# Optimization experiments

Hardware: AMD Instinct MI355X
Metric: run time of the kernel (lower is better)

Reference implementation:

```python
import jax, jax.numpy as jnp
import numpy as np

NH, NL, NP, GA = 8, 4, 4, 8  # num_heads, num_levels, num_points, grid_align_num
SHAPES = np.array([[128, 128], [64, 64], [32, 32], [16, 16]], dtype=np.int64)  # (W, H) per level


def _grid_sample(img, grid):
    """F.grid_sample bilinear, padding_mode='zeros', align_corners=False.
    img: [N,C,H,W], grid: [N,Hg,Wg,2] in [-1,1] (x,y). Returns [N,C,Hg,Wg]."""
    N, C, H, W = img.shape
    x = (grid[..., 0] + 1.0) * (W * 0.5) - 0.5
    y = (grid[..., 1] + 1.0) * (H * 0.5) - 0.5
    x0 = jnp.floor(x)
    y0 = jnp.floor(y)
    wx = (x - x0)[:, None]  # [N,1,Hg,Wg]
    wy = (y - y0)[:, None]
    x0i = x0.astype(jnp.int32)
    y0i = y0.astype(jnp.int32)
    img_flat = img.reshape(N, C, H * W)
    Hg, Wg = grid.shape[1], grid.shape[2]

    def tap(ix, iy):
        valid = (ix >= 0) & (ix < W) & (iy >= 0) & (iy < H)
        lin = jnp.clip(iy, 0, H - 1) * W + jnp.clip(ix, 0, W - 1)
        v = jnp.take_along_axis(img_flat, lin.reshape(N, 1, Hg * Wg), axis=2)
        return v.reshape(N, C, Hg, Wg) * valid[:, None].astype(img.dtype)

    v00 = tap(x0i, y0i)
    v01 = tap(x0i + 1, y0i)
    v10 = tap(x0i, y0i + 1)
    v11 = tap(x0i + 1, y0i + 1)
    return (v00 * (1 - wx) * (1 - wy) + v01 * wx * (1 - wy)
            + v10 * (1 - wx) * wy + v11 * wx * wy)


def setup_inputs() -> dict:
    key = jax.random.key(0)
    ks = jax.random.split(key, 6)
    bs, nq, E = 2, 16384, 256
    total = int((SHAPES[:, 0] * SHAPES[:, 1]).sum())  # 21760
    query = jax.random.normal(ks[0], (bs, nq, E), jnp.float32)
    value = jax.random.normal(ks[1], (bs, total, NH, E // NH), jnp.float32)
    reference_points = jax.random.uniform(ks[2], (bs, nq, 1, NL * 2), jnp.float32)
    W_off = jax.random.normal(ks[3], (NH * NL * NP * 2, E), jnp.float32) * 0.01
    # structured offset bias per init_weights (directional rays, radius ~ point index)
    thetas = jnp.arange(NH, dtype=jnp.float32) * (2.0 * np.pi / NH)
    gi = jnp.stack([jnp.cos(thetas), jnp.sin(thetas)], -1)  # [NH,2]
    gi = gi / jnp.max(jnp.abs(gi), axis=-1, keepdims=True)
    gi = jnp.tile(gi[:, None, None, :], (1, NL, NP, 1))
    gi = gi * jnp.arange(1, NP + 1, dtype=jnp.float32)[None, None, :, None]
    b_off = gi.reshape(-1)
    W_attn = jax.random.normal(ks[4], (NH * NL * NP, E), jnp.float32) * 0.01
    b_attn = jax.random.normal(ks[5], (NH * NL * NP,), jnp.float32) * 0.01
    return {"query": query, "value": value, "reference_points": reference_points,
            "W_off": W_off, "b_off": b_off, "W_attn": W_attn, "b_attn": b_attn,
            "spatial_shapes": np.asarray(SHAPES)}


def reference(query, value, reference_points, W_off, b_off, W_attn, b_attn, spatial_shapes):
    bs, nq, E = query.shape
    d = E // NH
    shapes = np.asarray(spatial_shapes)  # static [L,2] (W,H)

    # sampling offsets and locations (non-deploy path)
    off = (query @ W_off.T + b_off).reshape(bs, nq, NH, NL * NP * 2)
    ref = jnp.tile(reference_points, (1, 1, NH, NP)).reshape(bs, nq, NH, NL * NP * 2)
    # offset_normalizer: (1/spatial_shapes).repeat(1, NP).flatten() -> layout (l, p, xy)
    norm = jnp.asarray(np.tile(1.0 / shapes.astype(np.float32), (1, NP)).reshape(-1))
    loc = (ref + off * norm) * 2.0 - 1.0  # [bs, nq, NH, NL*NP*2]

    # attention weights: softmax over levels*points, regrouped to (L, G, P) layout
    attn = jax.nn.softmax((query @ W_attn.T + b_attn).reshape(bs, nq, NH, NL * NP), axis=-1)
    attn = (attn.reshape(bs, nq // GA, GA, NH, NL, NP)
            .transpose(0, 3, 1, 4, 2, 5)
            .reshape(bs * NH, 1, nq // GA, NL * GA * NP))

    grids = loc.reshape(bs, nq, NH, NL, NP, 2)
    outs = []
    start = 0
    for lvl in range(NL):
        W_, H_ = int(shapes[lvl, 0]), int(shapes[lvl, 1])
        n = H_ * W_
        v = value[:, start:start + n].transpose(0, 2, 3, 1).reshape(bs * NH, d, H_, W_)
        start += n
        g = grids[:, :, :, lvl].transpose(0, 2, 1, 3, 4).reshape(bs * NH, nq // GA, GA * NP, 2)
        outs.append(_grid_sample(v, g))  # [bs*NH, d, nq//GA, GA*NP]
    samp = jnp.concatenate(outs, axis=-1) * attn  # [bs*NH, d, nq//GA, NL*GA*NP]
    # reduce_sum linear with fixed 0/1 weight == sum over levels and points per group slot
    out = samp.reshape(bs * NH, d, nq // GA, NL, GA, NP).sum(axis=(3, 5))
    return out.reshape(bs, NH * d, nq)
```

## Files before the change

kernel.cpp:

```cpp
#include <hip/hip_runtime.h>
#include <hip/hip_bf16.h>


typedef __attribute__((ext_vector_type(4))) float    float4v;
typedef __attribute__((ext_vector_type(8))) _Float16 half8;
typedef __attribute__((ext_vector_type(4))) _Float16 half4;

#define NQ    16384
#define NTOK  21760
#define NLOG  384

#define N_V4  2785280
#define N_W4  24576

__global__ __launch_bounds__(256) void convert_kernel(
    const float* __restrict__ val,
    const float* __restrict__ Woff, const float* __restrict__ Wattn,
    _Float16* __restrict__ vh, _Float16* __restrict__ wh) {
  int i = blockIdx.x * 256 + threadIdx.x;
  float4v v;
  half4* dst;
  if (i < N_V4) {
    v = ((const float4v*)val)[i];
    dst = ((half4*)vh) + i;
  } else {
    int j = i - N_V4;
    int n = j >> 6;
    int k4 = j & 63;
    const float* src = (n < 256) ? (Woff + (size_t)n * 256)
                                 : (Wattn + (size_t)(n - 256) * 256);
    v = *(const float4v*)(src + k4 * 4);
    dst = ((half4*)wh) + j;
  }
  half4 o;
  o[0] = (_Float16)v[0]; o[1] = (_Float16)v[1];
  o[2] = (_Float16)v[2]; o[3] = (_Float16)v[3];
  *dst = o;
}

#define LDSTR 88
__global__ __launch_bounds__(256) void gemm_kernel(
    const float* __restrict__ qf, const _Float16* __restrict__ wh,
    const float* __restrict__ boff, const float* __restrict__ battn,
    float* __restrict__ logits) {
  __shared__ _Float16 As[128 * LDSTR];
  __shared__ _Float16 Bs[128 * LDSTR];

  const int tid  = threadIdx.x;
  const int lane = tid & 63;
  const int wv   = tid >> 6;
  const int wm   = wv >> 1, wn = wv & 1;
  const int quad = lane >> 4;
  const int r    = lane & 15;
  const int blockM = blockIdx.x * 128;
  const int n0     = blockIdx.y * 128;

  float4v acc[4][4];
#pragma unroll
  for (int i = 0; i < 4; ++i)
#pragma unroll
    for (int j = 0; j < 4; ++j) acc[i][j] = (float4v){0.f, 0.f, 0.f, 0.f};

  for (int kc = 0; kc < 4; ++kc) {
    const int k0 = kc * 64;
    if (kc) __syncthreads();
#pragma unroll
    for (int it = 0; it < 8; ++it) {
      int idx = it * 256 + tid;
      int row = idx >> 4, k4 = idx & 15;
      float4v v = *(const float4v*)(qf + (size_t)(blockM + row) * 256 + k0 + k4 * 4);
      half4 o;
      o[0] = (_Float16)v[0]; o[1] = (_Float16)v[1];
      o[2] = (_Float16)v[2]; o[3] = (_Float16)v[3];
      *(half4*)&As[row * LDSTR + k4 * 4] = o;
    }
#pragma unroll
    for (int it = 0; it < 4; ++it) {
      int idx = it * 256 + tid;
      int row = idx >> 3, c8 = idx & 7;
      *(half8*)&Bs[row * LDSTR + c8 * 8] =
          *(const half8*)(wh + (size_t)(n0 + row) * 256 + k0 + c8 * 8);
    }
    __syncthreads();

#pragma unroll
    for (int kf = 0; kf < 2; ++kf) {
      const int ko = kf * 32 + quad * 8;
      half8 af[4], bf[4];
#pragma unroll
      for (int mi = 0; mi < 4; ++mi)
        af[mi] = *(const half8*)&As[(wm * 64 + mi * 16 + r) * LDSTR + ko];
#pragma unroll
      for (int ni = 0; ni < 4; ++ni)
        bf[ni] = *(const half8*)&Bs[(wn * 64 + ni * 16 + r) * LDSTR + ko];
#pragma unroll
      for (int mi = 0; mi < 4; ++mi)
#pragma unroll
        for (int ni = 0; ni < 4; ++ni)
          acc[mi][ni] = __builtin_amdgcn_mfma_f32_16x16x32_f16(af[mi], bf[ni], acc[mi][ni], 0, 0, 0);
    }
  }

#pragma unroll
  for (int mi = 0; mi < 4; ++mi) {
    const int mb = blockM + wm * 64 + mi * 16 + quad * 4;
#pragma unroll
    for (int ni = 0; ni < 4; ++ni) {
      const int n = n0 + wn * 64 + ni * 16 + r;
      const float bias = (n < 256) ? boff[n] : battn[n - 256];
#pragma unroll
      for (int reg = 0; reg < 4; ++reg)
        logits[(size_t)(mb + reg) * NLOG + n] = acc[mi][ni][reg] + bias;
    }
  }
}

__global__ __launch_bounds__(256) void sample_kernel(
    const _Float16* __restrict__ vh, const float* __restrict__ refp,
    const float* __restrict__ logits, float* __restrict__ out) {
  const int qt = blockIdx.x, h = blockIdx.y, b = blockIdx.z;
  const int tid = threadIdx.x;
  const int c4 = tid & 3;
  const int qi = tid >> 2;
  const int q  = qt * 64 + qi;
  const size_t bq = (size_t)b * NQ + q;
  const float* lg = logits + bq * NLOG;

  float4v al4[4];
#pragma unroll
  for (int i = 0; i < 4; ++i)
    al4[i] = *(const float4v*)(lg + 256 + h * 16 + i * 4);
  float mx = -1e30f;
#pragma unroll
  for (int i = 0; i < 4; ++i)
#pragma unroll
    for (int j = 0; j < 4; ++j) mx = fmaxf(mx, al4[i][j]);
  float ssum = 0.f;
#pragma unroll
  for (int i = 0; i < 4; ++i)
#pragma unroll
    for (int j = 0; j < 4; ++j) {
      float e = __expf(al4[i][j] - mx);
      al4[i][j] = e;
      ssum += e;
    }
  const float inv = 1.0f / ssum;

  float4v offv[8];
#pragma unroll
  for (int i = 0; i < 8; ++i)
    offv[i] = *(const float4v*)(lg + h * 32 + i * 4);
  float4v rp0 = *(const float4v*)(refp + bq * 8);
  float4v rp1 = *(const float4v*)(refp + bq * 8 + 4);
  const float rpx[4] = {rp0[0], rp0[2], rp1[0], rp1[2]};
  const float rpy[4] = {rp0[1], rp0[3], rp1[1], rp1[3]};

  const _Float16* vb = vh + (size_t)b * NTOK * 256 + h * 32 + c4 * 8;
  float4v acc0 = (float4v){0.f, 0.f, 0.f, 0.f};
  float4v acc1 = (float4v){0.f, 0.f, 0.f, 0.f};

  const int base[4] = {0, 16384, 20480, 21504};

#pragma unroll
  for (int l = 0; l < 4; ++l) {
    const int   W  = 128 >> l;
    const float fW = (float)W;
    const _Float16* vlev = vb + (size_t)base[l] * 256;
#pragma unroll
    for (int p = 0; p < 4; ++p) {
      const float a  = al4[l][p] * inv;
      const float ox = offv[l * 2 + (p >> 1)][(p & 1) * 2];
      const float oy = offv[l * 2 + (p >> 1)][(p & 1) * 2 + 1];
      const float x = rpx[p] * fW + ox - 0.5f;
      const float y = rpy[p] * fW + oy - 0.5f;
      const float xf = floorf(x), yf = floorf(y);
      const float fx = x - xf, fy = y - yf;
      const int ix = (int)xf, iy = (int)yf;
      const int ix0 = min(max(ix, 0), W - 1);
      const int ix1 = min(max(ix + 1, 0), W - 1);
      const int iy0 = min(max(iy, 0), W - 1);
      const int iy1 = min(max(iy + 1, 0), W - 1);
      const float wx0 = ((unsigned)ix       < (unsigned)W) ? 1.f - fx : 0.f;
      const float wx1 = ((unsigned)(ix + 1) < (unsigned)W) ? fx       : 0.f;
      const float wy0 = ((unsigned)iy       < (unsigned)W) ? 1.f - fy : 0.f;
      const float wy1 = ((unsigned)(iy + 1) < (unsigned)W) ? fy       : 0.f;
      const float w00 = a * wx0 * wy0, w01 = a * wx1 * wy0;
      const float w10 = a * wx0 * wy1, w11 = a * wx1 * wy1;
      const _Float16* r0 = vlev + (size_t)(iy0 * W) * 256;
      const _Float16* r1 = vlev + (size_t)(iy1 * W) * 256;
      half8 t00 = *(const half8*)(r0 + ix0 * 256);
      half8 t01 = *(const half8*)(r0 + ix1 * 256);
      half8 t10 = *(const half8*)(r1 + ix0 * 256);
      half8 t11 = *(const half8*)(r1 + ix1 * 256);
#pragma unroll
      for (int j = 0; j < 4; ++j) {
        acc0[j] += w00 * (float)t00[j]     + w01 * (float)t01[j]
                 + w10 * (float)t10[j]     + w11 * (float)t11[j];
        acc1[j] += w00 * (float)t00[j + 4] + w01 * (float)t01[j + 4]
                 + w10 * (float)t10[j + 4] + w11 * (float)t11[j + 4];
      }
    }
  }

  __shared__ float sm[32][65];
#pragma unroll
  for (int j = 0; j < 4; ++j) {
    sm[c4 * 8 + j][qi]     = acc0[j];
    sm[c4 * 8 + 4 + j][qi] = acc1[j];
  }
  __syncthreads();
  const size_t obase = ((size_t)b * 256 + h * 32) * NQ + qt * 64;
#pragma unroll
  for (int i = 0; i < 8; ++i) {
    const int idx = i * 256 + tid;
    const int c = idx >> 6, qq = idx & 63;
    out[obase + (size_t)c * NQ + qq] = sm[c][qq];
  }
}

extern "C" void kernel_launch(void* const* d_in, const int* in_sizes, int n_in,
                              void* d_out, int out_size, void* d_ws, size_t ws_size,
                              hipStream_t stream) {
  const float* query = (const float*)d_in[0];
  const float* value = (const float*)d_in[1];
  const float* refp  = (const float*)d_in[2];
  const float* Woff  = (const float*)d_in[3];
  const float* boff  = (const float*)d_in[4];
  const float* Wattn = (const float*)d_in[5];
  const float* battn = (const float*)d_in[6];
  float* out = (float*)d_out;

  char* ws = (char*)d_ws;
  _Float16* vh     = (_Float16*)ws;
  _Float16* wh     = (_Float16*)(ws + 22282240);
  float*    logits = (float*)(ws + 22478848);

  convert_kernel<<<10976, 256, 0, stream>>>(value, Woff, Wattn, vh, wh);
  gemm_kernel<<<dim3(256, 3), 256, 0, stream>>>(query, wh, boff, battn, logits);
  sample_kernel<<<dim3(256, 8, 2), 256, 0, stream>>>(vh, refp, logits, out);
}
```

Before: 228.4 us.

## Store logits in fp16, accumulate bilinear taps in packed half, shrink GEMM tile

The GEMM now writes its logits as fp16 instead of fp32, which halves the logit traffic between the GEMM and the sampling kernel. The GEMM converts the weights to fp16 inline, so the weight conversion pass in convert_kernel goes away, and its M tile drops from 128 to 64 to launch twice as many blocks. The sampling kernel does the per-level bilinear accumulation with packed half2 multiply-adds and converts to fp32 once per level. These changes are meant to cut memory traffic and ALU work, at the cost of lower precision in the offsets and the sampled accumulations.

```diff
diff --git a/kernel.cpp b/kernel.cpp
--- a/kernel.cpp
+++ b/kernel.cpp
@@ -5,45 +5,33 @@
 typedef __attribute__((ext_vector_type(4))) float    float4v;
 typedef __attribute__((ext_vector_type(8))) _Float16 half8;
 typedef __attribute__((ext_vector_type(4))) _Float16 half4;
+typedef __attribute__((ext_vector_type(2))) _Float16 half2v;
 
 #define NQ    16384
 #define NTOK  21760
 #define NLOG  384
 
 #define N_V4  2785280
-#define N_W4  24576
+
+union H8 { half8 v; half2v p[4]; };
 
 __global__ __launch_bounds__(256) void convert_kernel(
-    const float* __restrict__ val,
-    const float* __restrict__ Woff, const float* __restrict__ Wattn,
-    _Float16* __restrict__ vh, _Float16* __restrict__ wh) {
+    const float* __restrict__ val, _Float16* __restrict__ vh) {
   int i = blockIdx.x * 256 + threadIdx.x;
-  float4v v;
-  half4* dst;
-  if (i < N_V4) {
-    v = ((const float4v*)val)[i];
-    dst = ((half4*)vh) + i;
-  } else {
-    int j = i - N_V4;
-    int n = j >> 6;
-    int k4 = j & 63;
-    const float* src = (n < 256) ? (Woff + (size_t)n * 256)
-                                 : (Wattn + (size_t)(n - 256) * 256);
-    v = *(const float4v*)(src + k4 * 4);
-    dst = ((half4*)wh) + j;
-  }
+  float4v v = ((const float4v*)val)[i];
   half4 o;
   o[0] = (_Float16)v[0]; o[1] = (_Float16)v[1];
   o[2] = (_Float16)v[2]; o[3] = (_Float16)v[3];
-  *dst = o;
+  ((half4*)vh)[i] = o;
 }
 
 #define LDSTR 88
 __global__ __launch_bounds__(256) void gemm_kernel(
-    const float* __restrict__ qf, const _Float16* __restrict__ wh,
+    const float* __restrict__ qf,
+    const float* __restrict__ Woff, const float* __restrict__ Wattn,
     const float* __restrict__ boff, const float* __restrict__ battn,
-    float* __restrict__ logits) {
-  __shared__ _Float16 As[128 * LDSTR];
+    _Float16* __restrict__ lh) {
+  __shared__ _Float16 As[64 * LDSTR];
   __shared__ _Float16 Bs[128 * LDSTR];
 
   const int tid  = threadIdx.x;
@@ -52,12 +40,12 @@
   const int wm   = wv >> 1, wn = wv & 1;
   const int quad = lane >> 4;
   const int r    = lane & 15;
-  const int blockM = blockIdx.x * 128;
+  const int blockM = blockIdx.x * 64;
   const int n0     = blockIdx.y * 128;
 
-  float4v acc[4][4];
-#pragma unroll
-  for (int i = 0; i < 4; ++i)
+  float4v acc[2][4];
+#pragma unroll
+  for (int i = 0; i < 2; ++i)
 #pragma unroll
     for (int j = 0; j < 4; ++j) acc[i][j] = (float4v){0.f, 0.f, 0.f, 0.f};
 
@@ -65,7 +53,7 @@
     const int k0 = kc * 64;
     if (kc) __syncthreads();
 #pragma unroll
-    for (int it = 0; it < 8; ++it) {
+    for (int it = 0; it < 4; ++it) {
       int idx = it * 256 + tid;
       int row = idx >> 4, k4 = idx & 15;
       float4v v = *(const float4v*)(qf + (size_t)(blockM + row) * 256 + k0 + k4 * 4);
@@ -75,26 +63,32 @@
       *(half4*)&As[row * LDSTR + k4 * 4] = o;
     }
 #pragma unroll
-    for (int it = 0; it < 4; ++it) {
+    for (int it = 0; it < 8; ++it) {
       int idx = it * 256 + tid;
-      int row = idx >> 3, c8 = idx & 7;
-      *(half8*)&Bs[row * LDSTR + c8 * 8] =
-          *(const half8*)(wh + (size_t)(n0 + row) * 256 + k0 + c8 * 8);
+      int row = idx >> 4, k4 = idx & 15;
+      int n = n0 + row;
+      const float* src = (n < 256) ? (Woff + (size_t)n * 256)
+                                   : (Wattn + (size_t)(n - 256) * 256);
+      float4v v = *(const float4v*)(src + k0 + k4 * 4);
+      half4 o;
+      o[0] = (_Float16)v[0]; o[1] = (_Float16)v[1];
+      o[2] = (_Float16)v[2]; o[3] = (_Float16)v[3];
+      *(half4*)&Bs[row * LDSTR + k4 * 4] = o;
     }
     __syncthreads();
 
 #pragma unroll
     for (int kf = 0; kf < 2; ++kf) {
       const int ko = kf * 32 + quad * 8;
-      half8 af[4], bf[4];
-#pragma unroll
-      for (int mi = 0; mi < 4; ++mi)
-        af[mi] = *(const half8*)&As[(wm * 64 + mi * 16 + r) * LDSTR + ko];
+      half8 af[2], bf[4];
+#pragma unroll
+      for (int mi = 0; mi < 2; ++mi)
+        af[mi] = *(const half8*)&As[(wm * 32 + mi * 16 + r) * LDSTR + ko];
 #pragma unroll
       for (int ni = 0; ni < 4; ++ni)
         bf[ni] = *(const half8*)&Bs[(wn * 64 + ni * 16 + r) * LDSTR + ko];
 #pragma unroll
-      for (int mi = 0; mi < 4; ++mi)
+      for (int mi = 0; mi < 2; ++mi)
 #pragma unroll
         for (int ni = 0; ni < 4; ++ni)
           acc[mi][ni] = __builtin_amdgcn_mfma_f32_16x16x32_f16(af[mi], bf[ni], acc[mi][ni], 0, 0, 0);
@@ -102,54 +96,56 @@
   }
 
 #pragma unroll
-  for (int mi = 0; mi < 4; ++mi) {
-    const int mb = blockM + wm * 64 + mi * 16 + quad * 4;
+  for (int mi = 0; mi < 2; ++mi) {
+    const int mb = blockM + wm * 32 + mi * 16 + quad * 4;
 #pragma unroll
     for (int ni = 0; ni < 4; ++ni) {
       const int n = n0 + wn * 64 + ni * 16 + r;
       const float bias = (n < 256) ? boff[n] : battn[n - 256];
 #pragma unroll
       for (int reg = 0; reg < 4; ++reg)
-        logits[(size_t)(mb + reg) * NLOG + n] = acc[mi][ni][reg] + bias;
+        lh[(size_t)(mb + reg) * NLOG + n] = (_Float16)(acc[mi][ni][reg] + bias);
     }
   }
 }
 
 __global__ __launch_bounds__(256) void sample_kernel(
     const _Float16* __restrict__ vh, const float* __restrict__ refp,
-    const float* __restrict__ logits, float* __restrict__ out) {
+    const _Float16* __restrict__ lh, float* __restrict__ out) {
   const int qt = blockIdx.x, h = blockIdx.y, b = blockIdx.z;
   const int tid = threadIdx.x;
   const int c4 = tid & 3;
   const int qi = tid >> 2;
   const int q  = qt * 64 + qi;
   const size_t bq = (size_t)b * NQ + q;
-  const float* lg = logits + bq * NLOG;
-
-  float4v al4[4];
-#pragma unroll
-  for (int i = 0; i < 4; ++i)
-    al4[i] = *(const float4v*)(lg + 256 + h * 16 + i * 4);
+  const _Float16* lg = lh + bq * NLOG;
+
+  float offf[32];
+#pragma unroll
+  for (int i = 0; i < 4; ++i) {
+    half8 oh = *(const half8*)(lg + h * 32 + i * 8);
+#pragma unroll
+    for (int j = 0; j < 8; ++j) offf[i * 8 + j] = (float)oh[j];
+  }
+  float al[16];
+#pragma unroll
+  for (int i = 0; i < 2; ++i) {
+    half8 ah = *(const half8*)(lg + 256 + h * 16 + i * 8);
+#pragma unroll
+    for (int j = 0; j < 8; ++j) al[i * 8 + j] = (float)ah[j];
+  }
   float mx = -1e30f;
 #pragma unroll
-  for (int i = 0; i < 4; ++i)
-#pragma unroll
-    for (int j = 0; j < 4; ++j) mx = fmaxf(mx, al4[i][j]);
+  for (int i = 0; i < 16; ++i) mx = fmaxf(mx, al[i]);
   float ssum = 0.f;
 #pragma unroll
-  for (int i = 0; i < 4; ++i)
-#pragma unroll
-    for (int j = 0; j < 4; ++j) {
-      float e = __expf(al4[i][j] - mx);
-      al4[i][j] = e;
-      ssum += e;
-    }
+  for (int i = 0; i < 16; ++i) {
+    float e = __expf(al[i] - mx);
+    al[i] = e;
+    ssum += e;
+  }
   const float inv = 1.0f / ssum;
 
-  float4v offv[8];
-#pragma unroll
-  for (int i = 0; i < 8; ++i)
-    offv[i] = *(const float4v*)(lg + h * 32 + i * 4);
   float4v rp0 = *(const float4v*)(refp + bq * 8);
   float4v rp1 = *(const float4v*)(refp + bq * 8 + 4);
   const float rpx[4] = {rp0[0], rp0[2], rp1[0], rp1[2]};
@@ -166,11 +162,14 @@
     const int   W  = 128 >> l;
     const float fW = (float)W;
     const _Float16* vlev = vb + (size_t)base[l] * 256;
+    half2v accl[4];
+#pragma unroll
+    for (int j = 0; j < 4; ++j) accl[j] = (half2v){(_Float16)0, (_Float16)0};
 #pragma unroll
     for (int p = 0; p < 4; ++p) {
-      const float a  = al4[l][p] * inv;
-      const float ox = offv[l * 2 + (p >> 1)][(p & 1) * 2];
-      const float oy = offv[l * 2 + (p >> 1)][(p & 1) * 2 + 1];
+      const float a  = al[l * 4 + p] * inv;
+      const float ox = offf[l * 8 + p * 2];
+      const float oy = offf[l * 8 + p * 2 + 1];
       const float x = rpx[p] * fW + ox - 0.5f;
       const float y = rpy[p] * fW + oy - 0.5f;
       const float xf = floorf(x), yf = floorf(y);
@@ -184,22 +183,31 @@
       const float wx1 = ((unsigned)(ix + 1) < (unsigned)W) ? fx       : 0.f;
       const float wy0 = ((unsigned)iy       < (unsigned)W) ? 1.f - fy : 0.f;
       const float wy1 = ((unsigned)(iy + 1) < (unsigned)W) ? fy       : 0.f;
-      const float w00 = a * wx0 * wy0, w01 = a * wx1 * wy0;
-      const float w10 = a * wx0 * wy1, w11 = a * wx1 * wy1;
+      const _Float16 w00 = (_Float16)(a * wx0 * wy0);
+      const _Float16 w01 = (_Float16)(a * wx1 * wy0);
+      const _Float16 w10 = (_Float16)(a * wx0 * wy1);
+      const _Float16 w11 = (_Float16)(a * wx1 * wy1);
+      const half2v h00 = (half2v){w00, w00};
+      const half2v h01 = (half2v){w01, w01};
+      const half2v h10 = (half2v){w10, w10};
+      const half2v h11 = (half2v){w11, w11};
       const _Float16* r0 = vlev + (size_t)(iy0 * W) * 256;
       const _Float16* r1 = vlev + (size_t)(iy1 * W) * 256;
-      half8 t00 = *(const half8*)(r0 + ix0 * 256);
-      half8 t01 = *(const half8*)(r0 + ix1 * 256);
-      half8 t10 = *(const half8*)(r1 + ix0 * 256);
-      half8 t11 = *(const half8*)(r1 + ix1 * 256);
+      H8 t00, t01, t10, t11;
+      t00.v = *(const half8*)(r0 + ix0 * 256);
+      t01.v = *(const half8*)(r0 + ix1 * 256);
+      t10.v = *(const half8*)(r1 + ix0 * 256);
+      t11.v = *(const half8*)(r1 + ix1 * 256);
 #pragma unroll
       for (int j = 0; j < 4; ++j) {
-        acc0[j] += w00 * (float)t00[j]     + w01 * (float)t01[j]
-                 + w10 * (float)t10[j]     + w11 * (float)t11[j];
-        acc1[j] += w00 * (float)t00[j + 4] + w01 * (float)t01[j + 4]
-                 + w10 * (float)t10[j + 4] + w11 * (float)t11[j + 4];
+        accl[j] += h00 * t00.p[j] + h01 * t01.p[j]
+                 + h10 * t10.p[j] + h11 * t11.p[j];
       }
     }
+    acc0[0] += (float)accl[0][0]; acc0[1] += (float)accl[0][1];
+    acc0[2] += (float)accl[1][0]; acc0[3] += (float)accl[1][1];
+    acc1[0] += (float)accl[2][0]; acc1[1] += (float)accl[2][1];
+    acc1[2] += (float)accl[3][0]; acc1[3] += (float)accl[3][1];
   }
 
   __shared__ float sm[32][65];
@@ -231,11 +239,10 @@
   float* out = (float*)d_out;
 
   char* ws = (char*)d_ws;
-  _Float16* vh     = (_Float16*)ws;
-  _Float16* wh     = (_Float16*)(ws + 22282240);
-  float*    logits = (float*)(ws + 22478848);
-
-  convert_kernel<<<10976, 256, 0, stream>>>(value, Woff, Wattn, vh, wh);
-  gemm_kernel<<<dim3(256, 3), 256, 0, stream>>>(query, wh, boff, battn, logits);
-  sample_kernel<<<dim3(256, 8, 2), 256, 0, stream>>>(vh, refp, logits, out);
-}
+  _Float16* vh = (_Float16*)ws;
+  _Float16* lh = (_Float16*)(ws + 22282240);
+
+  convert_kernel<<<10880, 256, 0, stream>>>(value, vh);
+  gemm_kernel<<<dim3(512, 3), 256, 0, stream>>>(query, Woff, Wattn, boff, battn, lh);
+  sample_kernel<<<dim3(256, 8, 2), 256, 0, stream>>>(vh, refp, lh, out);
+}
```

Result: slower. 239.1 us (+4.7%).
